# Kernel tuning notes

Hardware: AMD Instinct MI355X
Metric: run time of the kernel (lower is better)

Reference implementation:

```python
import jax, jax.numpy as jnp
import numpy as np

DIM = 512
NUM_HEADS = 8
HEAD_DIM = DIM // NUM_HEADS
EPS = 1e-6


def setup_inputs() -> dict:
    key = jax.random.key(0)
    k_x, k_qkv, k_out, k_b = jax.random.split(key, 4)
    B, N = 8, 4096
    x = jax.random.normal(k_x, (B, N, DIM), dtype=jnp.float32)
    # nn.Linear weights stored as [out_features, in_features]; we keep [in, out] for x @ W
    s_qkv = 1.0 / np.sqrt(DIM)
    W_qkv = jax.random.uniform(k_qkv, (DIM, 3 * DIM), minval=-s_qkv, maxval=s_qkv, dtype=jnp.float32)
    W_out = jax.random.uniform(k_out, (DIM, DIM), minval=-s_qkv, maxval=s_qkv, dtype=jnp.float32)
    b_out = jax.random.uniform(k_b, (DIM,), minval=-s_qkv, maxval=s_qkv, dtype=jnp.float32)
    return {"x": x, "W_qkv": W_qkv, "W_out": W_out, "b_out": b_out}


def _feature_map(x):
    # elu(x) + 1
    return jax.nn.elu(x) + 1.0


def reference(x, W_qkv, W_out, b_out):
    B, N, C = x.shape
    H, D = NUM_HEADS, HEAD_DIM
    qkv = x @ W_qkv                              # [B, N, 3C]
    qkv = qkv.reshape(B, N, 3, H, D).transpose(2, 0, 3, 1, 4)  # [3, B, H, N, D]
    q, k, v = qkv[0], qkv[1], qkv[2]
    q_phi = _feature_map(q)                      # [B, H, N, D]
    k_phi = _feature_map(k)
    KV = jnp.einsum('bhnd,bhne->bhde', k_phi, v)  # [B, H, D, D]
    K_sum = k_phi.sum(axis=2)                     # [B, H, D]
    denom = jnp.einsum('bhnd,bhd->bhn', q_phi, K_sum)[..., None] + EPS  # [B, H, N, 1]
    out = jnp.einsum('bhnd,bhde->bhne', q_phi, KV) / denom              # [B, H, N, D]
    out = out.transpose(0, 2, 1, 3).reshape(B, N, C)
    return out @ W_out + b_out
```

## Files before the change

kernel.cpp:

```cpp
#include <hip/hip_runtime.h>
#include <stdint.h>

typedef float    f32x4 __attribute__((ext_vector_type(4)));
typedef short    s16x8 __attribute__((ext_vector_type(8)));
typedef short    s16x4 __attribute__((ext_vector_type(4)));
typedef unsigned short u16;
typedef uint32_t u32;

#define DEVINL __device__ __forceinline__

DEVINL float bf2f(u16 u) { union { u32 i; float f; } x; x.i = ((u32)u) << 16; return x.f; }
DEVINL u16 f2bf(float f) {
  union { float f; u32 i; } x; x.f = f;
  u32 i = x.i;
  return (u16)((i + 0x7FFFu + ((i >> 16) & 1u)) >> 16);
}

DEVINL void gload16(const void* g, void* l) {
  __builtin_amdgcn_global_load_lds((const __attribute__((address_space(1))) void*)g,
                                   (__attribute__((address_space(3))) void*)l,
                                   16, 0, 0);
}

__global__ __launch_bounds__(256) void k_conv_bf16(const float* __restrict__ x,
                                                   u16* __restrict__ xb, int n8) {
  int stride = gridDim.x * blockDim.x;
  for (int i = blockIdx.x * blockDim.x + threadIdx.x; i < n8; i += stride) {
    const f32x4* p = (const f32x4*)(x + (size_t)i * 8);
    f32x4 a = p[0], b = p[1];
    s16x8 o;
    o[0] = (short)f2bf(a[0]); o[1] = (short)f2bf(a[1]);
    o[2] = (short)f2bf(a[2]); o[3] = (short)f2bf(a[3]);
    o[4] = (short)f2bf(b[0]); o[5] = (short)f2bf(b[1]);
    o[6] = (short)f2bf(b[2]); o[7] = (short)f2bf(b[3]);
    *(s16x8*)(xb + (size_t)i * 8) = o;
  }
}

__global__ __launch_bounds__(256) void k_transpose_bf16(const float* __restrict__ W,
                                                        u16* __restrict__ Wt, int K, int N) {
  __shared__ __align__(16) float t[64][65];
  int nb = N >> 6;
  int tn = blockIdx.x % nb, tk = blockIdx.x / nb;
  int n0 = tn << 6, k0 = tk << 6;
  int tid = threadIdx.x;
  int cr = tid >> 4, cc = (tid & 15) << 2;
#pragma unroll
  for (int i = 0; i < 4; i++) {
    int r = cr + (i << 4);
    f32x4 v = *(const f32x4*)(W + (size_t)(k0 + r) * N + n0 + cc);
    t[r][cc] = v[0]; t[r][cc + 1] = v[1]; t[r][cc + 2] = v[2]; t[r][cc + 3] = v[3];
  }
  __syncthreads();
#pragma unroll
  for (int i = 0; i < 4; i++) {
    int nn = cr + (i << 4);
    s16x4 o;
    o[0] = (short)f2bf(t[cc    ][nn]);
    o[1] = (short)f2bf(t[cc + 1][nn]);
    o[2] = (short)f2bf(t[cc + 2][nn]);
    o[3] = (short)f2bf(t[cc + 3][nn]);
    *(s16x4*)(Wt + (size_t)(n0 + nn) * K + k0 + cc) = o;
  }
}

template <int EPI>
__global__ __launch_bounds__(512, 2) void k_gemm(
    const u16* __restrict__ A, const u16* __restrict__ Bt,
    int nbn,
    u16* __restrict__ qph, u16* __restrict__ kph, u16* __restrict__ vv,
    float* __restrict__ out, const float* __restrict__ bias) {
  __shared__ __align__(16) u16 lsA[4][256 * 32];
  __shared__ __align__(16) u16 lsB[4][256 * 32];

  int nwg = gridDim.x;
  int bx = blockIdx.x;
  int o = (bx & 7) * (nwg >> 3) + (bx >> 3);
  int bm = o / nbn, bn = o % nbn;
  int m0 = bm << 8, n0 = bn << 8;
  int tid = threadIdx.x;
  int w = tid >> 6, lane = tid & 63;
  int lnlo = lane & 15, lnhi = lane >> 4;
  int wr = w >> 2, wc = w & 3;

  int c1 = tid + 512;
  int r0 = tid >> 2, r1 = c1 >> 2;
  int ch0 = (tid & 3) ^ ((r0 >> 1) & 3);
  int ch1 = (c1 & 3) ^ ((r1 >> 1) & 3);
  const u16* gA0 = A + (size_t)(m0 + r0) * 512 + ch0 * 8;
  const u16* gA1 = A + (size_t)(m0 + r1) * 512 + ch1 * 8;
  const u16* gB0 = Bt + (size_t)(n0 + r0) * 512 + ch0 * 8;
  const u16* gB1 = Bt + (size_t)(n0 + r1) * 512 + ch1 * 8;

  int offA[8], offB[4];
#pragma unroll
  for (int f = 0; f < 8; f++) {
    int r = wr * 128 + f * 16 + lnlo;
    offA[f] = (r * 4 + (lnhi ^ ((r >> 1) & 3))) * 8;
  }
#pragma unroll
  for (int f = 0; f < 4; f++) {
    int r = wc * 64 + f * 16 + lnlo;
    offB[f] = (r * 4 + (lnhi ^ ((r >> 1) & 3))) * 8;
  }

  auto stage = [&](int s) {
    int buf = s & 3, k0 = s * 32;
    gload16(gA0 + k0, &lsA[buf][tid * 8]);
    gload16(gA1 + k0, &lsA[buf][c1 * 8]);
    gload16(gB0 + k0, &lsB[buf][tid * 8]);
    gload16(gB1 + k0, &lsB[buf][c1 * 8]);
  };

  f32x4 acc[8][4] = {};

  stage(0); stage(1); stage(2);
  asm volatile("s_waitcnt vmcnt(8)" ::: "memory");
  __builtin_amdgcn_s_barrier();
  __builtin_amdgcn_sched_barrier(0);

#pragma unroll
  for (int s = 0; s < 16; s++) {
    int buf = s & 3;
    s16x8 af[8], bf[4];
#pragma unroll
    for (int f = 0; f < 8; f++) af[f] = *(const s16x8*)&lsA[buf][offA[f]];
#pragma unroll
    for (int f = 0; f < 4; f++) bf[f] = *(const s16x8*)&lsB[buf][offB[f]];
    if (s < 13) stage(s + 3);
    __builtin_amdgcn_s_barrier();
    __builtin_amdgcn_sched_barrier(0);
    asm volatile("s_waitcnt lgkmcnt(0)" ::: "memory");
    __builtin_amdgcn_sched_barrier(0);
    __builtin_amdgcn_s_setprio(1);
#pragma unroll
    for (int mf = 0; mf < 8; mf++)
#pragma unroll
      for (int nf = 0; nf < 4; nf++)
        acc[mf][nf] = __builtin_amdgcn_mfma_f32_16x16x32_bf16(af[mf], bf[nf], acc[mf][nf], 0, 0, 0);
    __builtin_amdgcn_s_setprio(0);
    __builtin_amdgcn_sched_barrier(0);
    if (s <= 12)      asm volatile("s_waitcnt vmcnt(8)" ::: "memory");
    else if (s == 13) asm volatile("s_waitcnt vmcnt(4)" ::: "memory");
    else if (s == 14) asm volatile("s_waitcnt vmcnt(0)" ::: "memory");
    if (s < 15) {
      __builtin_amdgcn_s_barrier();
      __builtin_amdgcn_sched_barrier(0);
    }
  }

  int gmB = m0 + wr * 128;
  int gnB = n0 + wc * 64;
  if (EPI == 0) {
#pragma unroll
    for (int mf = 0; mf < 8; mf++) {
#pragma unroll
      for (int nf = 0; nf < 4; nf++) {
        int col = gnB + nf * 16 + lnlo;
        int sec = col >> 9;
        int hh = (col >> 6) & 7;
        int dd = col & 63;
        u16* dst = (sec == 0) ? qph : ((sec == 1) ? kph : vv);
#pragma unroll
        for (int r = 0; r < 4; r++) {
          int rowm = gmB + mf * 16 + lnhi * 4 + r;
          float val = acc[mf][nf][r];
          if (sec < 2) val = (val > 0.f) ? (val + 1.f) : __expf(val);
          int bidx = rowm >> 12, tok = rowm & 4095;
          dst[(((size_t)(bidx * 8 + hh) * 4096 + tok) << 6) + dd] = f2bf(val);
        }
      }
    }
  } else {
#pragma unroll
    for (int mf = 0; mf < 8; mf++) {
#pragma unroll
      for (int nf = 0; nf < 4; nf++) {
        int col = gnB + nf * 16 + lnlo;
        float bv = bias[col];
#pragma unroll
        for (int r = 0; r < 4; r++) {
          int rowm = gmB + mf * 16 + lnhi * 4 + r;
          out[(size_t)rowm * 512 + col] = acc[mf][nf][r] + bv;
        }
      }
    }
  }
}

__global__ __launch_bounds__(256) void k_kv(const u16* __restrict__ kphi,
                                            const u16* __restrict__ vbuf,
                                            float* __restrict__ kvpart,
                                            float* __restrict__ kspart) {
  __shared__ __align__(16) float kf[16][64];
  __shared__ __align__(16) float vf[16][64];
  int bx = blockIdx.x;
  int bh = bx >> 4, ck = bx & 15;
  int tid = threadIdx.x;
  size_t base = ((size_t)bh * 4096 + ck * 256) * 64;
  float acc[4][4] = {};
  float ks[4] = {0.f, 0.f, 0.f, 0.f};
  int dq = tid >> 4, eq = tid & 15;
  int d0 = dq * 4, e0 = eq * 4;
  int half = tid >> 7;
  int t2 = tid & 127;
  int srow = t2 >> 3, sch = t2 & 7;

  for (int step = 0; step < 16; step++) {
    {
      const u16* src = (half ? vbuf : kphi) + base + (size_t)(step * 16 + srow) * 64 + sch * 8;
      s16x8 v8 = *(const s16x8*)src;
      float* dst = (half ? &vf[0][0] : &kf[0][0]) + srow * 64 + sch * 8;
      f32x4 lo = {bf2f((u16)v8[0]), bf2f((u16)v8[1]), bf2f((u16)v8[2]), bf2f((u16)v8[3])};
      f32x4 hi = {bf2f((u16)v8[4]), bf2f((u16)v8[5]), bf2f((u16)v8[6]), bf2f((u16)v8[7])};
      *(f32x4*)dst = lo;
      *(f32x4*)(dst + 4) = hi;
    }
    __syncthreads();
#pragma unroll
    for (int tk = 0; tk < 16; tk++) {
      f32x4 kq = *(const f32x4*)&kf[tk][d0];
      f32x4 vq = *(const f32x4*)&vf[tk][e0];
#pragma unroll
      for (int i = 0; i < 4; i++)
#pragma unroll
        for (int j = 0; j < 4; j++) acc[i][j] += kq[i] * vq[j];
      if (eq == 0) {
#pragma unroll
        for (int i = 0; i < 4; i++) ks[i] += kq[i];
      }
    }
    __syncthreads();
  }
  size_t pb = (size_t)(bh * 16 + ck) * 4096;
#pragma unroll
  for (int i = 0; i < 4; i++) {
    f32x4 o = {acc[i][0], acc[i][1], acc[i][2], acc[i][3]};
    *(f32x4*)(kvpart + pb + (size_t)(d0 + i) * 64 + e0) = o;
  }
  if (eq == 0) {
    f32x4 o = {ks[0], ks[1], ks[2], ks[3]};
    *(f32x4*)(kspart + (size_t)(bh * 16 + ck) * 64 + d0) = o;
  }
}

__global__ __launch_bounds__(256) void k_kvred(const float* __restrict__ kvpart,
                                               const float* __restrict__ kspart,
                                               u16* __restrict__ kvt_sw,
                                               float* __restrict__ ksum) {
  int bh = blockIdx.x;
  int tid = threadIdx.x;
  int e = tid >> 2, d0 = (tid & 3) * 16;
  size_t pb = (size_t)bh * 16 * 4096;
#pragma unroll
  for (int dd = 0; dd < 16; dd++) {
    int d = d0 + dd;
    float s = 0.f;
#pragma unroll
    for (int c = 0; c < 16; c++) s += kvpart[pb + (size_t)c * 4096 + d * 64 + e];
    int chs = (d >> 3) ^ (e & 7);
    kvt_sw[((size_t)bh * 64 + e) * 64 + chs * 8 + (d & 7)] = f2bf(s);
  }
  if (tid < 64) {
    float s = 0.f;
#pragma unroll
    for (int c = 0; c < 16; c++) s += kspart[(size_t)bh * 1024 + c * 64 + tid];
    ksum[bh * 64 + tid] = s;
  }
}

__global__ __launch_bounds__(256, 2) void k_attnout(const u16* __restrict__ qphi,
                                                    const u16* __restrict__ kvt_sw,
                                                    const float* __restrict__ ksum,
                                                    u16* __restrict__ y) {
  __shared__ __align__(16) u16 qa[256 * 64];
  __shared__ __align__(16) u16 bb[64 * 64];
  __shared__ float ksl[64];
  __shared__ float rdnl[256];
  int bx = blockIdx.x;
  int bh = bx >> 4, tch = bx & 15;
  int b = bh >> 3, hh = bh & 7;
  int tid = threadIdx.x, w = tid >> 6, lane = tid & 63;
  int lnlo = lane & 15, lnhi = lane >> 4;
  size_t qbase = ((size_t)bh * 4096 + tch * 256) * 64;

#pragma unroll
  for (int i = 0; i < 8; i++) {
    int c = i * 256 + tid;
    int row = c >> 3, ch = c & 7;
    int gcol = (ch ^ (row & 7)) << 3;
    gload16(qphi + qbase + (size_t)row * 64 + gcol, &qa[c * 8]);
  }
#pragma unroll
  for (int i = 0; i < 2; i++) {
    int c = i * 256 + tid;
    gload16(kvt_sw + (size_t)bh * 4096 + c * 8, &bb[c * 8]);
  }
  if (tid < 64) ksl[tid] = ksum[bh * 64 + tid];
  __syncthreads();

  {
    float den = 0.f;
#pragma unroll
    for (int ch = 0; ch < 8; ch++) {
      s16x8 v8 = *(const s16x8*)&qa[tid * 64 + ((ch ^ (tid & 7)) << 3)];
#pragma unroll
      for (int j = 0; j < 8; j++) den += bf2f((u16)v8[j]) * ksl[ch * 8 + j];
    }
    rdnl[tid] = 1.f / (den + 1e-6f);
  }
  __syncthreads();

  f32x4 acc[4][4] = {};
#pragma unroll
  for (int kk = 0; kk < 2; kk++) {
    s16x8 af[4], bfr[4];
#pragma unroll
    for (int f = 0; f < 4; f++) {
      int ra = w * 64 + f * 16 + lnlo;
      int ca = (kk * 4 + lnhi) ^ (ra & 7);
      af[f] = *(const s16x8*)&qa[ra * 64 + ca * 8];
      int rb = f * 16 + lnlo;
      int cb = (kk * 4 + lnhi) ^ (rb & 7);
      bfr[f] = *(const s16x8*)&bb[rb * 64 + cb * 8];
    }
#pragma unroll
    for (int mf = 0; mf < 4; mf++)
#pragma unroll
      for (int nf = 0; nf < 4; nf++)
        acc[mf][nf] = __builtin_amdgcn_mfma_f32_16x16x32_bf16(af[mf], bfr[nf], acc[mf][nf], 0, 0, 0);
  }

  size_t yrow0 = (size_t)b * 4096 + tch * 256;
#pragma unroll
  for (int mf = 0; mf < 4; mf++) {
#pragma unroll
    for (int nf = 0; nf < 4; nf++) {
      int e = nf * 16 + lnlo;
#pragma unroll
      for (int r = 0; r < 4; r++) {
        int tl = w * 64 + mf * 16 + lnhi * 4 + r;
        float val = acc[mf][nf][r] * rdnl[tl];
        y[(yrow0 + tl) * 512 + hh * 64 + e] = f2bf(val);
      }
    }
  }
}

#define OFF_XB     ((size_t)0)
#define OFF_WQKVT  ((size_t)33554432)
#define OFF_WOUTT  ((size_t)35127296)
#define OFF_QPHI   ((size_t)35651584)
#define OFF_KPHI   ((size_t)69206016)
#define OFF_VBUF   ((size_t)102760448)
#define OFF_KVPART ((size_t)136314880)
#define OFF_KSPART ((size_t)153092096)
#define OFF_KVT    ((size_t)153354240)
#define OFF_KSUM   ((size_t)153878528)

extern "C" void kernel_launch(void* const* d_in, const int* in_sizes, int n_in,
                              void* d_out, int out_size, void* d_ws, size_t ws_size,
                              hipStream_t stream) {
  const float* x    = (const float*)d_in[0];
  const float* Wqkv = (const float*)d_in[1];
  const float* Wout = (const float*)d_in[2];
  const float* bout = (const float*)d_in[3];
  float* out = (float*)d_out;
  char* ws = (char*)d_ws;

  u16* xb     = (u16*)(ws + OFF_XB);
  u16* y      = (u16*)(ws + OFF_XB);
  u16* wqkvt  = (u16*)(ws + OFF_WQKVT);
  u16* woutt  = (u16*)(ws + OFF_WOUTT);
  u16* qphi   = (u16*)(ws + OFF_QPHI);
  u16* kphi   = (u16*)(ws + OFF_KPHI);
  u16* vbuf   = (u16*)(ws + OFF_VBUF);
  float* kvpart = (float*)(ws + OFF_KVPART);
  float* kspart = (float*)(ws + OFF_KSPART);
  u16* kvt_sw = (u16*)(ws + OFF_KVT);
  float* ksum = (float*)(ws + OFF_KSUM);

  k_conv_bf16<<<2048, 256, 0, stream>>>(x, xb, 16777216 / 8);
  k_transpose_bf16<<<(1536 / 64) * (512 / 64), 256, 0, stream>>>(Wqkv, wqkvt, 512, 1536);
  k_transpose_bf16<<<(512 / 64) * (512 / 64), 256, 0, stream>>>(Wout, woutt, 512, 512);

  k_gemm<0><<<768, 512, 0, stream>>>(xb, wqkvt, 6, qphi, kphi, vbuf, nullptr, nullptr);
  k_kv<<<64 * 16, 256, 0, stream>>>(kphi, vbuf, kvpart, kspart);
  k_kvred<<<64, 256, 0, stream>>>(kvpart, kspart, kvt_sw, ksum);
  k_attnout<<<64 * 16, 256, 0, stream>>>(qphi, kvt_sw, ksum, y);
  k_gemm<1><<<256, 512, 0, stream>>>(y, woutt, 2, nullptr, nullptr, nullptr, out, bout);
}
```

Measured before the change: 181.5 us.

## Switch GEMM to double-buffered BK=64 tiles with 8-way XOR swizzle

```diff
diff --git a/kernel.cpp b/kernel.cpp
--- a/kernel.cpp
+++ b/kernel.cpp
@@ -65,13 +65,13 @@
 }
 
 template <int EPI>
-__global__ __launch_bounds__(512, 2) void k_gemm(
+__global__ __launch_bounds__(512, 1) void k_gemm(
     const u16* __restrict__ A, const u16* __restrict__ Bt,
     int nbn,
     u16* __restrict__ qph, u16* __restrict__ kph, u16* __restrict__ vv,
     float* __restrict__ out, const float* __restrict__ bias) {
-  __shared__ __align__(16) u16 lsA[4][256 * 32];
-  __shared__ __align__(16) u16 lsB[4][256 * 32];
+  __shared__ __align__(16) u16 lsA[2][256 * 64];
+  __shared__ __align__(16) u16 lsB[2][256 * 64];
 
   int nwg = gridDim.x;
   int bx = blockIdx.x;
@@ -83,69 +83,69 @@
   int lnlo = lane & 15, lnhi = lane >> 4;
   int wr = w >> 2, wc = w & 3;
 
-  int c1 = tid + 512;
-  int r0 = tid >> 2, r1 = c1 >> 2;
-  int ch0 = (tid & 3) ^ ((r0 >> 1) & 3);
-  int ch1 = (c1 & 3) ^ ((r1 >> 1) & 3);
-  const u16* gA0 = A + (size_t)(m0 + r0) * 512 + ch0 * 8;
-  const u16* gA1 = A + (size_t)(m0 + r1) * 512 + ch1 * 8;
-  const u16* gB0 = Bt + (size_t)(n0 + r0) * 512 + ch0 * 8;
-  const u16* gB1 = Bt + (size_t)(n0 + r1) * 512 + ch1 * 8;
-
-  int offA[8], offB[4];
-#pragma unroll
-  for (int f = 0; f < 8; f++) {
-    int r = wr * 128 + f * 16 + lnlo;
-    offA[f] = (r * 4 + (lnhi ^ ((r >> 1) & 3))) * 8;
-  }
-#pragma unroll
-  for (int f = 0; f < 4; f++) {
-    int r = wc * 64 + f * 16 + lnlo;
-    offB[f] = (r * 4 + (lnhi ^ ((r >> 1) & 3))) * 8;
-  }
-
-  auto stage = [&](int s) {
-    int buf = s & 3, k0 = s * 32;
-    gload16(gA0 + k0, &lsA[buf][tid * 8]);
-    gload16(gA1 + k0, &lsA[buf][c1 * 8]);
-    gload16(gB0 + k0, &lsB[buf][tid * 8]);
-    gload16(gB1 + k0, &lsB[buf][c1 * 8]);
+  const u16* gAp[4]; const u16* gBp[4]; int ldst[4];
+#pragma unroll
+  for (int i = 0; i < 4; i++) {
+    int c = tid + i * 512;
+    int row = c >> 3, chl = c & 7;
+    int gch = chl ^ (row & 7);
+    gAp[i] = A + (size_t)(m0 + row) * 512 + gch * 8;
+    gBp[i] = Bt + (size_t)(n0 + row) * 512 + gch * 8;
+    ldst[i] = c * 8;
+  }
+
+  int offA[2][8], offB[2][4];
+#pragma unroll
+  for (int ks = 0; ks < 2; ks++) {
+#pragma unroll
+    for (int f = 0; f < 8; f++) {
+      int r = wr * 128 + f * 16 + lnlo;
+      offA[ks][f] = (r * 8 + ((ks * 4 + lnhi) ^ (r & 7))) * 8;
+    }
+#pragma unroll
+    for (int f = 0; f < 4; f++) {
+      int r = wc * 64 + f * 16 + lnlo;
+      offB[ks][f] = (r * 8 + ((ks * 4 + lnhi) ^ (r & 7))) * 8;
+    }
+  }
+
+  auto stage = [&](int t) {
+    int par = t & 1, k0 = t * 64;
+#pragma unroll
+    for (int i = 0; i < 4; i++) gload16(gAp[i] + k0, &lsA[par][ldst[i]]);
+#pragma unroll
+    for (int i = 0; i < 4; i++) gload16(gBp[i] + k0, &lsB[par][ldst[i]]);
   };
 
   f32x4 acc[8][4] = {};
 
-  stage(0); stage(1); stage(2);
-  asm volatile("s_waitcnt vmcnt(8)" ::: "memory");
+  stage(0);
+  asm volatile("s_waitcnt vmcnt(0)" ::: "memory");
   __builtin_amdgcn_s_barrier();
-  __builtin_amdgcn_sched_barrier(0);
-
-#pragma unroll
-  for (int s = 0; s < 16; s++) {
-    int buf = s & 3;
-    s16x8 af[8], bf[4];
-#pragma unroll
-    for (int f = 0; f < 8; f++) af[f] = *(const s16x8*)&lsA[buf][offA[f]];
-#pragma unroll
-    for (int f = 0; f < 4; f++) bf[f] = *(const s16x8*)&lsB[buf][offB[f]];
-    if (s < 13) stage(s + 3);
-    __builtin_amdgcn_s_barrier();
-    __builtin_amdgcn_sched_barrier(0);
-    asm volatile("s_waitcnt lgkmcnt(0)" ::: "memory");
-    __builtin_amdgcn_sched_barrier(0);
-    __builtin_amdgcn_s_setprio(1);
-#pragma unroll
-    for (int mf = 0; mf < 8; mf++)
-#pragma unroll
-      for (int nf = 0; nf < 4; nf++)
-        acc[mf][nf] = __builtin_amdgcn_mfma_f32_16x16x32_bf16(af[mf], bf[nf], acc[mf][nf], 0, 0, 0);
-    __builtin_amdgcn_s_setprio(0);
-    __builtin_amdgcn_sched_barrier(0);
-    if (s <= 12)      asm volatile("s_waitcnt vmcnt(8)" ::: "memory");
-    else if (s == 13) asm volatile("s_waitcnt vmcnt(4)" ::: "memory");
-    else if (s == 14) asm volatile("s_waitcnt vmcnt(0)" ::: "memory");
-    if (s < 15) {
+
+  for (int t = 0; t < 8; t++) {
+    int par = t & 1;
+    if (t < 7) stage(t + 1);
+    const u16* La = &lsA[par][0];
+    const u16* Lb = &lsB[par][0];
+#pragma unroll
+    for (int ks = 0; ks < 2; ks++) {
+      s16x8 af[8], bf[4];
+#pragma unroll
+      for (int f = 0; f < 8; f++) af[f] = *(const s16x8*)(La + offA[ks][f]);
+#pragma unroll
+      for (int f = 0; f < 4; f++) bf[f] = *(const s16x8*)(Lb + offB[ks][f]);
+      __builtin_amdgcn_s_setprio(1);
+#pragma unroll
+      for (int mf = 0; mf < 8; mf++)
+#pragma unroll
+        for (int nf = 0; nf < 4; nf++)
+          acc[mf][nf] = __builtin_amdgcn_mfma_f32_16x16x32_bf16(af[mf], bf[nf], acc[mf][nf], 0, 0, 0);
+      __builtin_amdgcn_s_setprio(0);
+    }
+    if (t < 7) {
+      asm volatile("s_waitcnt vmcnt(0)" ::: "memory");
       __builtin_amdgcn_s_barrier();
-      __builtin_amdgcn_sched_barrier(0);
     }
   }
 
```

Result: no change. 184.7 us (+1.8%).
